# Kernel tuning notes

Measured on AMD Instinct MI355X. Metric: run time of the kernel, lower is better.

Reference implementation:

```python
import jax, jax.numpy as jnp
import numpy as np

H = 64      # num_heads == num_key_value_heads == head_dim (forced by mask broadcast)
D = 64      # head_dim
HID = 4096  # hidden_size = H * D
B, S = 2, 4096


def setup_inputs() -> dict:
    key = jax.random.key(0)
    ks = jax.random.split(key, 8)
    s = 1.0 / np.sqrt(HID)
    return {
        "hidden_states": jax.random.normal(ks[0], (B, S, HID), jnp.float32),
        "Wq": jax.random.normal(ks[1], (HID, HID), jnp.float32) * s,
        "Wk": jax.random.normal(ks[2], (HID, HID), jnp.float32) * s,
        "Wv": jax.random.normal(ks[3], (HID, HID), jnp.float32) * s,
        "Wo": jax.random.normal(ks[4], (HID, HID), jnp.float32) * s,
        "mu_q": jnp.zeros((H,), jnp.float32),
        "sigma_q": jnp.ones((H,), jnp.float32) * 0.5,
        "mu_kv": jnp.zeros((H,), jnp.float32),
        "sigma_kv": jnp.ones((H,), jnp.float32) * 0.5,
        "eps_q": jax.random.normal(ks[5], (H,), jnp.float32),
        "eps_kv": jax.random.normal(ks[6], (H,), jnp.float32),
    }


def reference(hidden_states, Wq, Wk, Wv, Wo, mu_q, sigma_q, mu_kv, sigma_kv, eps_q, eps_kv):
    b, s, _ = hidden_states.shape
    # projections (Linear weight is [out, in] -> x @ W.T), reshape to [B,S,H,D]
    q = (hidden_states @ Wq.T).reshape(b, s, H, D)
    k = (hidden_states @ Wk.T).reshape(b, s, H, D)
    v = (hidden_states @ Wv.T).reshape(b, s, H, D)
    # VIB masks: 1-D length-H vector broadcast onto the LAST (head_dim) axis,
    # exactly as in the torch code (requires H == D).
    mask_q = jax.nn.sigmoid(mu_q + eps_q * sigma_q)    # [H]==[D]
    mask_kv = jax.nn.sigmoid(mu_kv + eps_kv * sigma_kv)
    q = q * mask_q
    k = k * mask_kv
    v = v * mask_kv
    # num_key_value_groups == 1 -> repeat is a no-op.
    # torch: matmul on [B,S,H,D] @ [B,S,D,H] -> per-token attention ACROSS HEADS
    scores = jnp.einsum('bshd,bsgd->bshg', q, k) / np.sqrt(D)  # [B,S,H,H]
    w = jax.nn.softmax(scores, axis=-1)
    out = jnp.einsum('bshg,bsgd->bshd', w, v)          # [B,S,H,D]
    out = out.reshape(b, s, HID)
    return out @ Wo.T
```

## Files before the change

### kernel.cpp

```cpp
#include <hip/hip_runtime.h>
#include <hip/hip_bf16.h>

using bf16 = __hip_bfloat16;
typedef __attribute__((ext_vector_type(8))) short short8;
typedef __attribute__((ext_vector_type(4))) float f32x4;

#define GAS(p) ((const __attribute__((address_space(1))) unsigned int*)(p))
#define LAS(p) ((__attribute__((address_space(3))) unsigned int*)(p))

__global__ __launch_bounds__(256)
void cast_f32_to_bf16(const float* __restrict__ in, bf16* __restrict__ out, int n) {
  const int stride = gridDim.x * blockDim.x * 4;
  for (int i = (blockIdx.x * blockDim.x + threadIdx.x) * 4; i < n; i += stride) {
    float4 v = *reinterpret_cast<const float4*>(in + i);
    bf16 b0 = __float2bfloat16(v.x);
    bf16 b1 = __float2bfloat16(v.y);
    bf16 b2 = __float2bfloat16(v.z);
    bf16 b3 = __float2bfloat16(v.w);
    ushort4 p;
    p.x = *reinterpret_cast<unsigned short*>(&b0);
    p.y = *reinterpret_cast<unsigned short*>(&b1);
    p.z = *reinterpret_cast<unsigned short*>(&b2);
    p.w = *reinterpret_cast<unsigned short*>(&b3);
    *reinterpret_cast<ushort4*>(out + i) = p;
  }
}

template <typename OutT, bool KMASK>
__global__ __launch_bounds__(512, 2)
void gemm256(const bf16* __restrict__ A, const bf16* __restrict__ B,
             OutT* __restrict__ C, int M, int N, int K,
             const float* __restrict__ mu_q, const float* __restrict__ sigma_q,
             const float* __restrict__ eps_q,
             const float* __restrict__ mu_kv, const float* __restrict__ sigma_kv,
             const float* __restrict__ eps_kv) {
  extern __shared__ char smem[];

  const int nwg = gridDim.x;
  const int cpx = nwg >> 3;
  const int bid = blockIdx.x;
  const int swz = (bid & 7) * cpx + (bid >> 3);
  const int ntn = N >> 8;
  const int tm = swz / ntn, tn = swz % ntn;
  const int row0 = tm << 8, col0 = tn << 8;

  const int t = threadIdx.x;
  const int wave = t >> 6, lane = t & 63;
  const int wm = wave >> 2, wn = wave & 3;
  const int fl = lane & 15, g4 = lane >> 4;
  const int ldsWave = wave << 10;

  const int srow = t >> 3;
  const int scol = ((t & 7) * 8) ^
                   (((srow & 2) << 4) | ((srow & 4) << 2) | (srow & 8));
  size_t aRow[2][2], bRow[2][2];
#pragma unroll
  for (int q = 0; q < 2; ++q)
#pragma unroll
    for (int j = 0; j < 2; ++j) {
      aRow[q][j] = (size_t)(row0 + j * 128 + q * 64 + srow) * K + scol;
      bRow[q][j] = (size_t)(col0 + (j * 2 + (t >> 8)) * 64 + q * 32 +
                            ((t >> 3) & 31)) * K + scol;
    }

  int aoff[4][2], boff[2][2];
#pragma unroll
  for (int m = 0; m < 4; ++m) {
    const int lr = wm * 64 + m * 16 + fl;
    const int x = ((lr & 2) << 5) | ((lr & 4) << 3) | ((lr & 8) << 1);
    aoff[m][0] = lr * 128 + ((g4 * 16) ^ x);
    aoff[m][1] = lr * 128 + ((64 + g4 * 16) ^ x);
  }
#pragma unroll
  for (int n = 0; n < 2; ++n) {
    const int lr = wn * 32 + n * 16 + fl;
    const int x = ((lr & 2) << 5) | ((lr & 4) << 3) | ((lr & 8) << 1);
    boff[n][0] = lr * 128 + ((g4 * 16) ^ x);
    boff[n][1] = lr * 128 + ((64 + g4 * 16) ^ x);
  }

  f32x4 acc[8][4];
#pragma unroll
  for (int m = 0; m < 8; ++m)
#pragma unroll
    for (int n = 0; n < 4; ++n) acc[m][n] = (f32x4)0.f;

#define STG_A(buf_, q_, kk_) do {                                             \
    __builtin_amdgcn_global_load_lds(GAS(A + aRow[q_][0] + (kk_)),            \
        LAS(smem + (buf_) * 32768 + (q_) * 16384 + ldsWave), 16, 0, 0);       \
    __builtin_amdgcn_global_load_lds(GAS(A + aRow[q_][1] + (kk_)),            \
        LAS(smem + (buf_) * 32768 + (q_) * 16384 + 8192 + ldsWave), 16, 0, 0);\
  } while (0)
#define STG_B(buf_, q_, kk_) do {                                             \
    __builtin_amdgcn_global_load_lds(GAS(B + bRow[q_][0] + (kk_)),            \
        LAS(smem + 65536 + (buf_) * 32768 + (q_) * 16384 + ldsWave), 16, 0, 0);\
    __builtin_amdgcn_global_load_lds(GAS(B + bRow[q_][1] + (kk_)),            \
        LAS(smem + 65536 + (buf_) * 32768 + (q_) * 16384 + 8192 + ldsWave),   \
        16, 0, 0);                                                            \
  } while (0)

  const int NT = K >> 6;
  STG_A(0, 0, 0); STG_B(0, 0, 0); STG_B(0, 1, 0); STG_A(0, 1, 0);

  short8 af[4][2], bfq0[2][2], bfq1[2][2];

  for (int tt = 0; tt < NT; ++tt) {
    const int cur = tt & 1, nxt = cur ^ 1;
    const size_t kk = (size_t)((tt + 1 < NT) ? ((tt + 1) << 6) : 0);
    const char* As0 = smem + cur * 32768;
    const char* As1 = As0 + 16384;
    const char* Bs0 = smem + 65536 + cur * 32768;
    const char* Bs1 = Bs0 + 16384;

    asm volatile("s_waitcnt vmcnt(4)" ::: "memory");
    __builtin_amdgcn_s_barrier();
    asm volatile("" ::: "memory");
#pragma unroll
    for (int m = 0; m < 4; ++m) {
      af[m][0] = *reinterpret_cast<const short8*>(As0 + aoff[m][0]);
      af[m][1] = *reinterpret_cast<const short8*>(As0 + aoff[m][1]);
    }
#pragma unroll
    for (int n = 0; n < 2; ++n) {
      bfq0[n][0] = *reinterpret_cast<const short8*>(Bs0 + boff[n][0]);
      bfq0[n][1] = *reinterpret_cast<const short8*>(Bs0 + boff[n][1]);
    }
    STG_A(nxt, 0, kk);
    __builtin_amdgcn_s_setprio(1);
#pragma unroll
    for (int m = 0; m < 4; ++m)
#pragma unroll
      for (int n = 0; n < 2; ++n) {
        acc[m][n] = __builtin_amdgcn_mfma_f32_16x16x32_bf16(af[m][0], bfq0[n][0], acc[m][n], 0, 0, 0);
        acc[m][n] = __builtin_amdgcn_mfma_f32_16x16x32_bf16(af[m][1], bfq0[n][1], acc[m][n], 0, 0, 0);
      }
    __builtin_amdgcn_s_setprio(0);

    asm volatile("s_waitcnt vmcnt(4)" ::: "memory");
    __builtin_amdgcn_s_barrier();
    asm volatile("" ::: "memory");
#pragma unroll
    for (int n = 0; n < 2; ++n) {
      bfq1[n][0] = *reinterpret_cast<const short8*>(Bs1 + boff[n][0]);
      bfq1[n][1] = *reinterpret_cast<const short8*>(Bs1 + boff[n][1]);
    }
    STG_B(nxt, 0, kk);
    __builtin_amdgcn_s_setprio(1);
#pragma unroll
    for (int m = 0; m < 4; ++m)
#pragma unroll
      for (int n = 0; n < 2; ++n) {
        acc[m][2 + n] = __builtin_amdgcn_mfma_f32_16x16x32_bf16(af[m][0], bfq1[n][0], acc[m][2 + n], 0, 0, 0);
        acc[m][2 + n] = __builtin_amdgcn_mfma_f32_16x16x32_bf16(af[m][1], bfq1[n][1], acc[m][2 + n], 0, 0, 0);
      }
    __builtin_amdgcn_s_setprio(0);

    asm volatile("s_waitcnt vmcnt(4)" ::: "memory");
    __builtin_amdgcn_s_barrier();
    asm volatile("" ::: "memory");
#pragma unroll
    for (int m = 0; m < 4; ++m) {
      af[m][0] = *reinterpret_cast<const short8*>(As1 + aoff[m][0]);
      af[m][1] = *reinterpret_cast<const short8*>(As1 + aoff[m][1]);
    }
    STG_B(nxt, 1, kk);
    __builtin_amdgcn_s_setprio(1);
#pragma unroll
    for (int m = 0; m < 4; ++m)
#pragma unroll
      for (int n = 0; n < 2; ++n) {
        acc[4 + m][n] = __builtin_amdgcn_mfma_f32_16x16x32_bf16(af[m][0], bfq0[n][0], acc[4 + m][n], 0, 0, 0);
        acc[4 + m][n] = __builtin_amdgcn_mfma_f32_16x16x32_bf16(af[m][1], bfq0[n][1], acc[4 + m][n], 0, 0, 0);
      }
    __builtin_amdgcn_s_setprio(0);

    STG_A(nxt, 1, kk);
    __builtin_amdgcn_s_setprio(1);
#pragma unroll
    for (int m = 0; m < 4; ++m)
#pragma unroll
      for (int n = 0; n < 2; ++n) {
        acc[4 + m][2 + n] = __builtin_amdgcn_mfma_f32_16x16x32_bf16(af[m][0], bfq1[n][0], acc[4 + m][2 + n], 0, 0, 0);
        acc[4 + m][2 + n] = __builtin_amdgcn_mfma_f32_16x16x32_bf16(af[m][1], bfq1[n][1], acc[4 + m][2 + n], 0, 0, 0);
      }
    __builtin_amdgcn_s_setprio(0);
  }
#undef STG_A
#undef STG_B

  asm volatile("s_waitcnt vmcnt(0)" ::: "memory");

  const int crow0 = row0 + wm * 128 + g4 * 4;
  const int ccol0 = col0 + wn * 64 + fl;
  float cscale[4];
  if constexpr (KMASK) {
#pragma unroll
    for (int n = 0; n < 4; ++n) {
      const int d = (ccol0 + n * 16) & 63;
      const float a = mu_q[d] + eps_q[d] * sigma_q[d];
      const float b = mu_kv[d] + eps_kv[d] * sigma_kv[d];
      cscale[n] = 0.125f / ((1.f + __expf(-a)) * (1.f + __expf(-b)));
    }
  }
#pragma unroll
  for (int m = 0; m < 8; ++m) {
#pragma unroll
    for (int n = 0; n < 4; ++n) {
      const int cc = ccol0 + n * 16;
#pragma unroll
      for (int r = 0; r < 4; ++r) {
        const int rr = crow0 + m * 16 + r;
        float v = acc[m][n][r];
        if constexpr (KMASK) v *= cscale[n];
        if constexpr (sizeof(OutT) == 2) {
          C[(size_t)rr * N + cc] = __float2bfloat16(v);
        } else {
          C[(size_t)rr * N + cc] = v;
        }
      }
    }
  }
}

__global__ __launch_bounds__(256)
void attn_mfma(const bf16* __restrict__ Q, const bf16* __restrict__ K,
               const bf16* __restrict__ V,
               const float* __restrict__ mu_kv, const float* __restrict__ sigma_kv,
               const float* __restrict__ eps_kv,
               bf16* __restrict__ AO) {
  __shared__ bf16 Vt[64][72];
  __shared__ bf16 P[4][16][72];

  const int t = threadIdx.x;
  const int wave = t >> 6, lane = t & 63;
  const int fl = lane & 15, g4 = lane >> 4;
  const int kq = g4 * 8;
  const size_t base = (size_t)blockIdx.x * 4096;

#pragma unroll
  for (int rep = 0; rep < 2; ++rep) {
    const int idx = rep * 256 + t;
    const int g = idx & 63;
    const int d0 = (idx >> 6) * 8;
    short8 v8 = *reinterpret_cast<const short8*>(&V[base + (size_t)g * 64 + d0]);
#pragma unroll
    for (int j = 0; j < 8; ++j)
      *reinterpret_cast<short*>(&Vt[d0 + j][g]) = (short)v8[j];
  }

  short8 aq[2];
#pragma unroll
  for (int ks = 0; ks < 2; ++ks)
    aq[ks] = *reinterpret_cast<const short8*>(
        &Q[base + (size_t)(wave * 16 + fl) * 64 + ks * 32 + kq]);
  short8 bk[4][2];
#pragma unroll
  for (int n = 0; n < 4; ++n)
#pragma unroll
    for (int ks = 0; ks < 2; ++ks)
      bk[n][ks] = *reinterpret_cast<const short8*>(
          &K[base + (size_t)(n * 16 + fl) * 64 + ks * 32 + kq]);

  f32x4 sacc[4];
#pragma unroll
  for (int n = 0; n < 4; ++n) sacc[n] = (f32x4)0.f;
#pragma unroll
  for (int n = 0; n < 4; ++n)
#pragma unroll
    for (int ks = 0; ks < 2; ++ks)
      sacc[n] = __builtin_amdgcn_mfma_f32_16x16x32_bf16(aq[ks], bk[n][ks],
                                                        sacc[n], 0, 0, 0);

  float recip[4];
  float ex[4][4];
#pragma unroll
  for (int r = 0; r < 4; ++r) {
    float mx = fmaxf(fmaxf(sacc[0][r], sacc[1][r]), fmaxf(sacc[2][r], sacc[3][r]));
    mx = fmaxf(mx, __shfl_xor(mx, 1, 64));
    mx = fmaxf(mx, __shfl_xor(mx, 2, 64));
    mx = fmaxf(mx, __shfl_xor(mx, 4, 64));
    mx = fmaxf(mx, __shfl_xor(mx, 8, 64));
    float sum = 0.f;
#pragma unroll
    for (int n = 0; n < 4; ++n) {
      ex[n][r] = __expf(sacc[n][r] - mx);
      sum += ex[n][r];
    }
    sum += __shfl_xor(sum, 1, 64);
    sum += __shfl_xor(sum, 2, 64);
    sum += __shfl_xor(sum, 4, 64);
    sum += __shfl_xor(sum, 8, 64);
    recip[r] = 1.f / sum;
  }

#pragma unroll
  for (int n = 0; n < 4; ++n)
#pragma unroll
    for (int r = 0; r < 4; ++r)
      P[wave][g4 * 4 + r][n * 16 + fl] = __float2bfloat16(ex[n][r]);

  __syncthreads();

  short8 ap[2];
#pragma unroll
  for (int ks = 0; ks < 2; ++ks)
    ap[ks] = *reinterpret_cast<const short8*>(&P[wave][fl][ks * 32 + kq]);
  short8 bv[4][2];
#pragma unroll
  for (int n = 0; n < 4; ++n)
#pragma unroll
    for (int ks = 0; ks < 2; ++ks)
      bv[n][ks] = *reinterpret_cast<const short8*>(&Vt[n * 16 + fl][ks * 32 + kq]);

  f32x4 oacc[4];
#pragma unroll
  for (int n = 0; n < 4; ++n) oacc[n] = (f32x4)0.f;
#pragma unroll
  for (int n = 0; n < 4; ++n)
#pragma unroll
    for (int ks = 0; ks < 2; ++ks)
      oacc[n] = __builtin_amdgcn_mfma_f32_16x16x32_bf16(ap[ks], bv[n][ks],
                                                        oacc[n], 0, 0, 0);

  float mkvc[4];
#pragma unroll
  for (int n = 0; n < 4; ++n) {
    const int d = n * 16 + fl;
    mkvc[n] = 1.f / (1.f + __expf(-(mu_kv[d] + eps_kv[d] * sigma_kv[d])));
  }
#pragma unroll
  for (int n = 0; n < 4; ++n) {
    const int d = n * 16 + fl;
#pragma unroll
    for (int r = 0; r < 4; ++r) {
      const int h = wave * 16 + g4 * 4 + r;
      AO[base + (size_t)h * 64 + d] =
          __float2bfloat16(oacc[n][r] * recip[r] * mkvc[n]);
    }
  }
}

extern "C" void kernel_launch(void* const* d_in, const int* in_sizes, int n_in,
                              void* d_out, int out_size, void* d_ws, size_t ws_size,
                              hipStream_t stream) {
  (void)in_sizes; (void)n_in; (void)out_size; (void)ws_size;
  const float* X        = (const float*)d_in[0];
  const float* Wq       = (const float*)d_in[1];
  const float* Wk       = (const float*)d_in[2];
  const float* Wv       = (const float*)d_in[3];
  const float* Wo       = (const float*)d_in[4];
  const float* mu_q     = (const float*)d_in[5];
  const float* sigma_q  = (const float*)d_in[6];
  const float* mu_kv    = (const float*)d_in[7];
  const float* sigma_kv = (const float*)d_in[8];
  const float* eps_q    = (const float*)d_in[9];
  const float* eps_kv   = (const float*)d_in[10];
  float* out = (float*)d_out;

  const int M = 8192, N = 4096, Kd = 4096;

  char* ws = (char*)d_ws;
  bf16* Xb = (bf16*)(ws);
  bf16* Wb = (bf16*)(ws + (size_t)64  * (1u << 20));
  bf16* Qb = (bf16*)(ws + (size_t)96  * (1u << 20));
  bf16* Kb = (bf16*)(ws + (size_t)160 * (1u << 20));
  bf16* Vb = (bf16*)(ws + (size_t)224 * (1u << 20));

  const int LDS_BYTES = 131072;
  hipFuncSetAttribute(reinterpret_cast<const void*>(&gemm256<bf16, false>),
                      hipFuncAttributeMaxDynamicSharedMemorySize, LDS_BYTES);
  hipFuncSetAttribute(reinterpret_cast<const void*>(&gemm256<bf16, true>),
                      hipFuncAttributeMaxDynamicSharedMemorySize, LDS_BYTES);
  hipFuncSetAttribute(reinterpret_cast<const void*>(&gemm256<float, false>),
                      hipFuncAttributeMaxDynamicSharedMemorySize, LDS_BYTES);

  const dim3 blk(256);
  const dim3 blk512(512);
  const dim3 cgrid(2048);
  const dim3 ggrid((M / 256) * (N / 256));

  cast_f32_to_bf16<<<cgrid, blk, 0, stream>>>(X, Xb, M * Kd);

  cast_f32_to_bf16<<<cgrid, blk, 0, stream>>>(Wq, Wb, N * Kd);
  gemm256<bf16, false><<<ggrid, blk512, LDS_BYTES, stream>>>(Xb, Wb, Qb, M, N, Kd,
      nullptr, nullptr, nullptr, nullptr, nullptr, nullptr);

  cast_f32_to_bf16<<<cgrid, blk, 0, stream>>>(Wk, Wb, N * Kd);
  gemm256<bf16, true><<<ggrid, blk512, LDS_BYTES, stream>>>(Xb, Wb, Kb, M, N, Kd,
      mu_q, sigma_q, eps_q, mu_kv, sigma_kv, eps_kv);

  cast_f32_to_bf16<<<cgrid, blk, 0, stream>>>(Wv, Wb, N * Kd);
  gemm256<bf16, false><<<ggrid, blk512, LDS_BYTES, stream>>>(Xb, Wb, Vb, M, N, Kd,
      nullptr, nullptr, nullptr, nullptr, nullptr, nullptr);

  bf16* AO = Xb;
  attn_mfma<<<dim3(M), blk, 0, stream>>>(Qb, Kb, Vb, mu_kv, sigma_kv, eps_kv, AO);

  cast_f32_to_bf16<<<cgrid, blk, 0, stream>>>(Wo, Wb, N * Kd);
  gemm256<float, false><<<ggrid, blk512, LDS_BYTES, stream>>>(AO, Wb, out, M, N, Kd,
      nullptr, nullptr, nullptr, nullptr, nullptr, nullptr);
}
```

Measured before the change: 1.077 ms.

## Prefetch LDS fragments for next quadrant ahead of MFMA in GEMM main loop

Restructures the GEMM K-loop so LDS fragment reads for the next sub-tile, including the first quadrant of the next K-step, are issued before the current MFMA block instead of at its start. A prologue preloads the first A/B fragments, and a second A-fragment register set (afA/afB) double-buffers operands. The vmcnt waits tighten from 4 to 2 to match the reordered global-to-LDS stages. The goal is to hide LDS read latency behind matrix math, at the cost of extra VGPRs and more delicate barrier/wait ordering.

```diff
diff --git a/kernel.cpp b/kernel.cpp
--- a/kernel.cpp
+++ b/kernel.cpp
@@ -102,86 +102,104 @@
   const int NT = K >> 6;
   STG_A(0, 0, 0); STG_B(0, 0, 0); STG_B(0, 1, 0); STG_A(0, 1, 0);
 
-  short8 af[4][2], bfq0[2][2], bfq1[2][2];
+  short8 afA[4][2], afB[4][2], bfq0[2][2], bfq1[2][2];
+
+  asm volatile("s_waitcnt vmcnt(4)" ::: "memory");
+  __builtin_amdgcn_s_barrier();
+  asm volatile("" ::: "memory");
+  {
+    const char* As0 = smem;
+    const char* Bs0 = smem + 65536;
+#pragma unroll
+    for (int m = 0; m < 4; ++m) {
+      afA[m][0] = *reinterpret_cast<const short8*>(As0 + aoff[m][0]);
+      afA[m][1] = *reinterpret_cast<const short8*>(As0 + aoff[m][1]);
+    }
+#pragma unroll
+    for (int n = 0; n < 2; ++n) {
+      bfq0[n][0] = *reinterpret_cast<const short8*>(Bs0 + boff[n][0]);
+      bfq0[n][1] = *reinterpret_cast<const short8*>(Bs0 + boff[n][1]);
+    }
+  }
 
   for (int tt = 0; tt < NT; ++tt) {
     const int cur = tt & 1, nxt = cur ^ 1;
     const size_t kk = (size_t)((tt + 1 < NT) ? ((tt + 1) << 6) : 0);
-    const char* As0 = smem + cur * 32768;
-    const char* As1 = As0 + 16384;
-    const char* Bs0 = smem + 65536 + cur * 32768;
-    const char* Bs1 = Bs0 + 16384;
-
-    asm volatile("s_waitcnt vmcnt(4)" ::: "memory");
+    const char* As1c = smem + cur * 32768 + 16384;
+    const char* Bs1c = smem + 65536 + cur * 32768 + 16384;
+    const char* As0n = smem + nxt * 32768;
+    const char* Bs0n = smem + 65536 + nxt * 32768;
+
+    asm volatile("s_waitcnt vmcnt(2)" ::: "memory");
     __builtin_amdgcn_s_barrier();
     asm volatile("" ::: "memory");
-#pragma unroll
-    for (int m = 0; m < 4; ++m) {
-      af[m][0] = *reinterpret_cast<const short8*>(As0 + aoff[m][0]);
-      af[m][1] = *reinterpret_cast<const short8*>(As0 + aoff[m][1]);
-    }
+    STG_A(nxt, 0, kk);
 #pragma unroll
     for (int n = 0; n < 2; ++n) {
-      bfq0[n][0] = *reinterpret_cast<const short8*>(Bs0 + boff[n][0]);
-      bfq0[n][1] = *reinterpret_cast<const short8*>(Bs0 + boff[n][1]);
-    }
-    STG_A(nxt, 0, kk);
+      bfq1[n][0] = *reinterpret_cast<const short8*>(Bs1c + boff[n][0]);
+      bfq1[n][1] = *reinterpret_cast<const short8*>(Bs1c + boff[n][1]);
+    }
     __builtin_amdgcn_s_setprio(1);
 #pragma unroll
     for (int m = 0; m < 4; ++m)
 #pragma unroll
       for (int n = 0; n < 2; ++n) {
-        acc[m][n] = __builtin_amdgcn_mfma_f32_16x16x32_bf16(af[m][0], bfq0[n][0], acc[m][n], 0, 0, 0);
-        acc[m][n] = __builtin_amdgcn_mfma_f32_16x16x32_bf16(af[m][1], bfq0[n][1], acc[m][n], 0, 0, 0);
+        acc[m][n] = __builtin_amdgcn_mfma_f32_16x16x32_bf16(afA[m][0], bfq0[n][0], acc[m][n], 0, 0, 0);
+        acc[m][n] = __builtin_amdgcn_mfma_f32_16x16x32_bf16(afA[m][1], bfq0[n][1], acc[m][n], 0, 0, 0);
       }
     __builtin_amdgcn_s_setprio(0);
 
-    asm volatile("s_waitcnt vmcnt(4)" ::: "memory");
+    asm volatile("s_waitcnt vmcnt(2)" ::: "memory");
     __builtin_amdgcn_s_barrier();
     asm volatile("" ::: "memory");
-#pragma unroll
-    for (int n = 0; n < 2; ++n) {
-      bfq1[n][0] = *reinterpret_cast<const short8*>(Bs1 + boff[n][0]);
-      bfq1[n][1] = *reinterpret_cast<const short8*>(Bs1 + boff[n][1]);
-    }
     STG_B(nxt, 0, kk);
+#pragma unroll
+    for (int m = 0; m < 4; ++m) {
+      afB[m][0] = *reinterpret_cast<const short8*>(As1c + aoff[m][0]);
+      afB[m][1] = *reinterpret_cast<const short8*>(As1c + aoff[m][1]);
+    }
     __builtin_amdgcn_s_setprio(1);
 #pragma unroll
     for (int m = 0; m < 4; ++m)
 #pragma unroll
       for (int n = 0; n < 2; ++n) {
-        acc[m][2 + n] = __builtin_amdgcn_mfma_f32_16x16x32_bf16(af[m][0], bfq1[n][0], acc[m][2 + n], 0, 0, 0);
-        acc[m][2 + n] = __builtin_amdgcn_mfma_f32_16x16x32_bf16(af[m][1], bfq1[n][1], acc[m][2 + n], 0, 0, 0);
+        acc[m][2 + n] = __builtin_amdgcn_mfma_f32_16x16x32_bf16(afA[m][0], bfq1[n][0], acc[m][2 + n], 0, 0, 0);
+        acc[m][2 + n] = __builtin_amdgcn_mfma_f32_16x16x32_bf16(afA[m][1], bfq1[n][1], acc[m][2 + n], 0, 0, 0);
       }
     __builtin_amdgcn_s_setprio(0);
 
-    asm volatile("s_waitcnt vmcnt(4)" ::: "memory");
+    STG_B(nxt, 1, kk);
+    __builtin_amdgcn_s_setprio(1);
+#pragma unroll
+    for (int m = 0; m < 4; ++m)
+#pragma unroll
+      for (int n = 0; n < 2; ++n) {
+        acc[4 + m][n] = __builtin_amdgcn_mfma_f32_16x16x32_bf16(afB[m][0], bfq0[n][0], acc[4 + m][n], 0, 0, 0);
+        acc[4 + m][n] = __builtin_amdgcn_mfma_f32_16x16x32_bf16(afB[m][1], bfq0[n][1], acc[4 + m][n], 0, 0, 0);
+      }
+    __builtin_amdgcn_s_setprio(0);
+
+    asm volatile("s_waitcnt vmcnt(2)" ::: "memory");
     __builtin_amdgcn_s_barrier();
     asm volatile("" ::: "memory");
+    STG_A(nxt, 1, kk);
 #pragma unroll
     for (int m = 0; m < 4; ++m) {
-      af[m][0] = *reinterpret_cast<const short8*>(As1 + aoff[m][0]);
-      af[m][1] = *reinterpret_cast<const short8*>(As1 + aoff[m][1]);
-    }
-    STG_B(nxt, 1, kk);
+      afA[m][0] = *reinterpret_cast<const short8*>(As0n + aoff[m][0]);
+      afA[m][1] = *reinterpret_cast<const short8*>(As0n + aoff[m][1]);
+    }
+#pragma unroll
+    for (int n = 0; n < 2; ++n) {
+      bfq0[n][0] = *reinterpret_cast<const short8*>(Bs0n + boff[n][0]);
+      bfq0[n][1] = *reinterpret_cast<const short8*>(Bs0n + boff[n][1]);
+    }
     __builtin_amdgcn_s_setprio(1);
 #pragma unroll
     for (int m = 0; m < 4; ++m)
 #pragma unroll
       for (int n = 0; n < 2; ++n) {
-        acc[4 + m][n] = __builtin_amdgcn_mfma_f32_16x16x32_bf16(af[m][0], bfq0[n][0], acc[4 + m][n], 0, 0, 0);
-        acc[4 + m][n] = __builtin_amdgcn_mfma_f32_16x16x32_bf16(af[m][1], bfq0[n][1], acc[4 + m][n], 0, 0, 0);
-      }
-    __builtin_amdgcn_s_setprio(0);
-
-    STG_A(nxt, 1, kk);
-    __builtin_amdgcn_s_setprio(1);
-#pragma unroll
-    for (int m = 0; m < 4; ++m)
-#pragma unroll
-      for (int n = 0; n < 2; ++n) {
-        acc[4 + m][2 + n] = __builtin_amdgcn_mfma_f32_16x16x32_bf16(af[m][0], bfq1[n][0], acc[4 + m][2 + n], 0, 0, 0);
-        acc[4 + m][2 + n] = __builtin_amdgcn_mfma_f32_16x16x32_bf16(af[m][1], bfq1[n][1], acc[4 + m][2 + n], 0, 0, 0);
+        acc[4 + m][2 + n] = __builtin_amdgcn_mfma_f32_16x16x32_bf16(afB[m][0], bfq1[n][0], acc[4 + m][2 + n], 0, 0, 0);
+        acc[4 + m][2 + n] = __builtin_amdgcn_mfma_f32_16x16x32_bf16(afB[m][1], bfq1[n][1], acc[4 + m][2 + n], 0, 0, 0);
       }
     __builtin_amdgcn_s_setprio(0);
   }
```

Result: no change. 1.076 ms (median of 2 runs) (-0.1%).
